# Kernel optimization log

Hardware: AMD Instinct MI355X
Metric: run time of the kernel (lower is better)

The kernel has to match this reference:

```python
import jax, jax.numpy as jnp
import numpy as np

N = 4096      # nodes
HID = 512     # hidden_size
HEADS = 8
DH = HID // HEADS
EPS = 1e-5    # BatchNorm eps


def setup_inputs() -> dict:
    key = jax.random.key(0)
    ks = jax.random.split(key, 16)
    h = jax.random.normal(ks[0], (N, HID), jnp.float32)
    # sparse adjacency (~degree 32) with self-loops so every row has a neighbor
    A = (jax.random.uniform(ks[1], (N, N)) < 0.008).astype(jnp.float32)
    A = jnp.maximum(A, jnp.eye(N, dtype=jnp.float32))
    w = lambda k, shp: jax.random.normal(k, shp, jnp.float32) * 0.02
    return {
        "A": A, "h": h,
        "Wq": w(ks[2], (HID, HID)), "bq": jnp.zeros((HID,), jnp.float32),
        "Wk": w(ks[3], (HID, HID)), "bk": jnp.zeros((HID,), jnp.float32),
        "Wv": w(ks[4], (HID, HID)), "bv": jnp.zeros((HID,), jnp.float32),
        "Wo": w(ks[5], (HID, HID)), "bo": jnp.zeros((HID,), jnp.float32),
        "bn1_g": jnp.ones((HID,), jnp.float32), "bn1_b": jnp.zeros((HID,), jnp.float32),
        "bn2_g": jnp.ones((HID,), jnp.float32), "bn2_b": jnp.zeros((HID,), jnp.float32),
        "W1": w(ks[6], (HID, 2 * HID)), "b1": jnp.zeros((2 * HID,), jnp.float32),
        "W2": w(ks[7], (2 * HID, HID)), "b2": jnp.zeros((HID,), jnp.float32),
    }


def _batchnorm(x, g, b):
    # BatchNorm1d training mode: stats over the node (batch) axis
    m = jnp.mean(x, axis=0)
    v = jnp.var(x, axis=0)
    return g * (x - m) * jax.lax.rsqrt(v + EPS) + b


def _layer(A, h, Wq, bq, Wk, bk, Wv, bv, Wo, bo,
           bn1_g, bn1_b, bn2_g, bn2_b, W1, b1, W2, b2):
    n = h.shape[0]
    q = (h @ Wq + bq).reshape(n, HEADS, DH)
    k = (h @ Wk + bk).reshape(n, HEADS, DH)
    v = (h @ Wv + bv).reshape(n, HEADS, DH)
    # scores [heads, n, m], masked by adjacency
    scores = jnp.einsum('nhd,mhd->hnm', q, k) / np.float32(np.sqrt(DH))
    scores = jnp.where(A[None, :, :] > 0, scores, jnp.float32(-1e9))
    attn = jax.nn.softmax(scores, axis=-1)
    o = jnp.einsum('hnm,mhd->nhd', attn, v).reshape(n, HID)
    h1 = o @ Wo + bo
    h = _batchnorm(h + h1, bn1_g, bn1_b)
    h2 = jax.nn.relu(h @ W1 + b1) @ W2 + b2
    return _batchnorm(h + h2, bn2_g, bn2_b)


def reference(A, h, Wq, bq, Wk, bk, Wv, bv, Wo, bo,
              bn1_g, bn1_b, bn2_g, bn2_b, W1, b1, W2, b2):
    return _layer(A, h, Wq, bq, Wk, bk, Wv, bv, Wo, bo,
                  bn1_g, bn1_b, bn2_g, bn2_b, W1, b1, W2, b2)
```

## Files before the change

kernel.cpp:

```cpp
#include <hip/hip_runtime.h>

#define N_NODES 4096
#define HID 512
#define HEADS 8
#define DH 64
#define EPS 1e-5f
#define MAXD 128

typedef __attribute__((ext_vector_type(8))) short bf16x8;
typedef __attribute__((ext_vector_type(4))) float f32x4;

__device__ __forceinline__ unsigned short f2bf(float f) {
    unsigned int u = __float_as_uint(f);
    unsigned int r = (u + 0x7FFFu + ((u >> 16) & 1u)) >> 16;
    return (unsigned short)r;
}
__device__ __forceinline__ float blo(unsigned int u) {
    return __uint_as_float(u << 16);
}
__device__ __forceinline__ float bhi(unsigned int u) {
    return __uint_as_float(u & 0xffff0000u);
}

__device__ __forceinline__ void gld_lds16(const void* g, void* l) {
    __builtin_amdgcn_global_load_lds(
        (const __attribute__((address_space(1))) unsigned int*)g,
        (__attribute__((address_space(3))) unsigned int*)l, 16, 0, 0);
}

template<int TM, int EPI>
__global__ __launch_bounds__(256) void gemm_bf16(
    const unsigned short* __restrict__ Xb, const unsigned short* __restrict__ Wt,
    const float* __restrict__ bias, const float* __restrict__ res,
    const unsigned short* __restrict__ resb,
    float* __restrict__ outf, unsigned short* __restrict__ outb,
    float* __restrict__ sum, float* __restrict__ sumsq,
    int K, int Nc)
{
    constexpr int WM = TM / 64;
    __shared__ __align__(16) unsigned short As[TM * 64];
    __shared__ __align__(16) unsigned short Bs[64 * 64];

    const int tid = threadIdx.x;
    const int lane = tid & 63;
    const int wv = tid >> 6;
    const int m0 = blockIdx.y * TM, n0 = blockIdx.x * 64;
    const int lc = lane & 15, lq = lane >> 4;
    const int rowbase = wv * (WM * 16);

    const int srow = tid >> 3;
    const int schunk = (tid & 7) ^ (srow & 7);
    unsigned short* ldsA = As + tid * 8;
    unsigned short* ldsB = Bs + tid * 8;
    const int rs0 = lq ^ (lc & 7);
    const int rs1 = (4 + lq) ^ (lc & 7);

    f32x4 acc[WM][4] = {};

    for (int k0 = 0; k0 < K; k0 += 64) {
        const unsigned short* gA = Xb + (size_t)(m0 + srow) * K + k0 + schunk * 8;
        const unsigned short* gB = Wt + (size_t)(n0 + srow) * K + k0 + schunk * 8;
        #pragma unroll
        for (int p = 0; p < TM / 32; ++p)
            gld_lds16(gA + (size_t)(p * 32) * K, ldsA + p * 2048);
        #pragma unroll
        for (int p = 0; p < 2; ++p)
            gld_lds16(gB + (size_t)(p * 32) * K, ldsB + p * 2048);
        __syncthreads();

        #pragma unroll
        for (int hh = 0; hh < 2; ++hh) {
            const int rs = hh ? rs1 : rs0;
            bf16x8 af[WM], bfr[4];
            #pragma unroll
            for (int i = 0; i < WM; ++i)
                af[i] = *(const bf16x8*)&As[(rowbase + i * 16 + lc) * 64 + rs * 8];
            #pragma unroll
            for (int j = 0; j < 4; ++j)
                bfr[j] = *(const bf16x8*)&Bs[(j * 16 + lc) * 64 + rs * 8];
            #pragma unroll
            for (int i = 0; i < WM; ++i)
                #pragma unroll
                for (int j = 0; j < 4; ++j)
                    acc[i][j] = __builtin_amdgcn_mfma_f32_16x16x32_bf16(af[i], bfr[j], acc[i][j], 0, 0, 0);
        }
        __syncthreads();
    }

    float cs[4] = {}, css[4] = {};
    #pragma unroll
    for (int i = 0; i < WM; ++i) {
        #pragma unroll
        for (int j = 0; j < 4; ++j) {
            const int gr0 = m0 + rowbase + i * 16 + lq * 4;
            const int gc = n0 + j * 16 + lc;
            const float bi = bias[gc];
            #pragma unroll
            for (int r = 0; r < 4; ++r) {
                float val = acc[i][j][r] + bi;
                size_t off = (size_t)(gr0 + r) * Nc + gc;
                if (EPI == 0)      outb[off] = f2bf(val);
                else if (EPI == 1) outb[off] = f2bf(fmaxf(val, 0.f));
                else {
                    if (EPI == 2) val += res[off];
                    else          val += blo((unsigned int)resb[off]);
                    outf[off] = val;
                    cs[j] += val; css[j] += val * val;
                }
            }
        }
    }
    if (EPI >= 2) {
        #pragma unroll
        for (int j = 0; j < 4; ++j) {
            float s = cs[j], ss = css[j];
            s += __shfl_xor(s, 16); s += __shfl_xor(s, 32);
            ss += __shfl_xor(ss, 16); ss += __shfl_xor(ss, 32);
            if (lq == 0) {
                const int gc = n0 + j * 16 + lc;
                atomicAdd(&sum[gc], s);
                atomicAdd(&sumsq[gc], ss);
            }
        }
    }
}

__global__ __launch_bounds__(256) void prep_all(
    const float* __restrict__ Wq, const float* __restrict__ Wk,
    const float* __restrict__ Wv, const float* __restrict__ Wo,
    const float* __restrict__ W1, const float* __restrict__ W2,
    const float* __restrict__ h,
    const float* __restrict__ bq, const float* __restrict__ bk,
    const float* __restrict__ bv,
    unsigned short* __restrict__ wqkvT, unsigned short* __restrict__ woT,
    unsigned short* __restrict__ w1T, unsigned short* __restrict__ w2T,
    unsigned int* __restrict__ hb, float* __restrict__ bqkv,
    float* __restrict__ st,
    const float* __restrict__ Adj, int* __restrict__ adjIdx,
    int* __restrict__ adjCnt)
{
    const int z = blockIdx.z;
    if (z < 6) {
        const float* in; unsigned short* out; int R, C;
        switch (z) {
            case 0: in = Wq; out = wqkvT;          R = 512;  C = 512;  break;
            case 1: in = Wk; out = wqkvT + 262144; R = 512;  C = 512;  break;
            case 2: in = Wv; out = wqkvT + 524288; R = 512;  C = 512;  break;
            case 3: in = Wo; out = woT;            R = 512;  C = 512;  break;
            case 4: in = W1; out = w1T;            R = 512;  C = 1024; break;
            default: in = W2; out = w2T;           R = 1024; C = 512;  break;
        }
        const int bc = blockIdx.x * 32, br = blockIdx.y * 32;
        if (bc >= C || br >= R) return;
        __shared__ float tile[32][33];
        const int tx = threadIdx.x & 31, ty = threadIdx.x >> 5;
        #pragma unroll
        for (int r = ty; r < 32; r += 8)
            tile[r][tx] = in[(size_t)(br + r) * C + bc + tx];
        __syncthreads();
        #pragma unroll
        for (int r = ty; r < 32; r += 8)
            out[(size_t)(bc + r) * R + br + tx] = f2bf(tile[tx][r]);
    } else if (z == 6) {
        const int blk = blockIdx.y * 32 + blockIdx.x;
        const int i = blk * 512 + threadIdx.x * 2;
        const float4* in4 = (const float4*)h;
        #pragma unroll
        for (int u = 0; u < 2; ++u) {
            float4 f = in4[i + u];
            hb[(i + u) * 2]     = (unsigned int)f2bf(f.x) | ((unsigned int)f2bf(f.y) << 16);
            hb[(i + u) * 2 + 1] = (unsigned int)f2bf(f.z) | ((unsigned int)f2bf(f.w) << 16);
        }
    } else if (z == 7) {
        const int blk = blockIdx.y * 32 + blockIdx.x;
        const int i = blk * 256 + threadIdx.x;
        if (i < 1536) bqkv[i] = i < 512 ? bq[i] : (i < 1024 ? bk[i - 512] : bv[i - 1024]);
        if (i < 2048) st[i] = 0.0f;
    } else {
        const int tid = threadIdx.x;
        const int lane = tid & 63;
        const int wv4 = tid >> 6;
        __shared__ int s_cnt[4];
        const unsigned long long lt = (1ull << lane) - 1ull;
        const int blk = blockIdx.y * 32 + blockIdx.x;
        #pragma unroll
        for (int it = 0; it < 4; ++it) {
            const int n = blk * 4 + it;
            const float4* r4 = (const float4*)(Adj + (size_t)n * N_NODES);
            float4 av[4];
            #pragma unroll
            for (int t = 0; t < 4; ++t)
                av[t] = r4[wv4 * 256 + t * 64 + lane];
            int cnt = 0;
            #pragma unroll
            for (int t = 0; t < 4; ++t) {
                #pragma unroll
                for (int b = 0; b < 4; ++b) {
                    float vb = (b == 0) ? av[t].x : (b == 1) ? av[t].y : (b == 2) ? av[t].z : av[t].w;
                    cnt += __popcll(__ballot(vb > 0.0f));
                }
            }
            if (lane == 0) s_cnt[wv4] = cnt;
            __syncthreads();
            int base = 0, total = 0;
            #pragma unroll
            for (int w = 0; w < 4; ++w) {
                if (w < wv4) base += s_cnt[w];
                total += s_cnt[w];
            }
            #pragma unroll
            for (int t = 0; t < 4; ++t) {
                #pragma unroll
                for (int b = 0; b < 4; ++b) {
                    float vb = (b == 0) ? av[t].x : (b == 1) ? av[t].y : (b == 2) ? av[t].z : av[t].w;
                    unsigned long long m = __ballot(vb > 0.0f);
                    if (vb > 0.0f) {
                        int p = base + __popcll(m & lt);
                        if (p < MAXD) adjIdx[n * MAXD + p] = wv4 * 1024 + t * 256 + lane * 4 + b;
                    }
                    base += __popcll(m);
                }
            }
            if (tid == 0) adjCnt[n] = total < MAXD ? total : MAXD;
            __syncthreads();
        }
    }
}

__global__ __launch_bounds__(256) void sparse_attn6(
    const int* __restrict__ adjIdx, const int* __restrict__ adjCnt,
    const unsigned short* __restrict__ qkv, unsigned short* __restrict__ o)
{
    const int n = blockIdx.x;
    const int tid = threadIdx.x;
    const int wv = tid >> 6, lane = tid & 63;

    __shared__ int s_idx[MAXD];
    __shared__ float s_p[8][MAXD];

    const int d = adjCnt[n];
    if (tid < d) s_idx[tid] = adjIdx[n * MAXD + tid];
    __syncthreads();

    const int jl = lane >> 3;
    const int dgs = lane & 7;
    const int jl2 = lane >> 4;
    const int dga = lane & 15;
    const int h0 = wv, h1 = wv + 4;

    const unsigned short* qp = qkv + (size_t)n * 1536 + dgs * 8;
    uint4 qa = *(const uint4*)(qp + h0 * 64);
    uint4 qb = *(const uint4*)(qp + h1 * 64);
    const float a0 = blo(qa.x), a1 = bhi(qa.x), a2 = blo(qa.y), a3 = bhi(qa.y);
    const float a4 = blo(qa.z), a5 = bhi(qa.z), a6 = blo(qa.w), a7 = bhi(qa.w);
    const float b0 = blo(qb.x), b1 = bhi(qb.x), b2 = blo(qb.y), b3 = bhi(qb.y);
    const float b4 = blo(qb.z), b5 = bhi(qb.z), b6 = blo(qb.w), b7 = bhi(qb.w);

    uint4 ka = {0, 0, 0, 0}, kb = {0, 0, 0, 0};
    if (jl < d) {
        const unsigned short* p = qkv + (size_t)s_idx[jl] * 1536 + 512 + dgs * 8;
        ka = *(const uint4*)(p + h0 * 64);
        kb = *(const uint4*)(p + h1 * 64);
    }
    for (int j0 = 0; j0 < d; j0 += 8) {
        const uint4 ca = ka, cb = kb;
        const int jn = j0 + 8 + jl;
        if (jn < d) {
            const unsigned short* p = qkv + (size_t)s_idx[jn] * 1536 + 512 + dgs * 8;
            ka = *(const uint4*)(p + h0 * 64);
            kb = *(const uint4*)(p + h1 * 64);
        }
        const int jc = j0 + jl;
        float s0 = 0.f, s1 = 0.f;
        if (jc < d) {
            s0 = a0 * blo(ca.x) + a1 * bhi(ca.x) + a2 * blo(ca.y) + a3 * bhi(ca.y)
               + a4 * blo(ca.z) + a5 * bhi(ca.z) + a6 * blo(ca.w) + a7 * bhi(ca.w);
            s1 = b0 * blo(cb.x) + b1 * bhi(cb.x) + b2 * blo(cb.y) + b3 * bhi(cb.y)
               + b4 * blo(cb.z) + b5 * bhi(cb.z) + b6 * blo(cb.w) + b7 * bhi(cb.w);
        }
        s0 += __shfl_xor(s0, 1); s1 += __shfl_xor(s1, 1);
        s0 += __shfl_xor(s0, 2); s1 += __shfl_xor(s1, 2);
        s0 += __shfl_xor(s0, 4); s1 += __shfl_xor(s1, 4);
        if (dgs == 0 && jc < d) {
            s_p[h0][jc] = s0 * 0.125f;
            s_p[h1][jc] = s1 * 0.125f;
        }
    }

    float inv0, inv1;
    #pragma unroll
    for (int hh = 0; hh < 2; ++hh) {
        float* sp = s_p[hh ? h1 : h0];
        float mx = -1e30f;
        for (int j = lane; j < d; j += 64) mx = fmaxf(mx, sp[j]);
        #pragma unroll
        for (int off = 32; off; off >>= 1) mx = fmaxf(mx, __shfl_xor(mx, off));
        float sum = 0.f;
        for (int j = lane; j < d; j += 64) {
            float e = __expf(sp[j] - mx);
            sp[j] = e;
            sum += e;
        }
        #pragma unroll
        for (int off = 32; off; off >>= 1) sum += __shfl_xor(sum, off);
        if (hh) inv1 = 1.0f / sum; else inv0 = 1.0f / sum;
    }

    float x0 = 0.f, x1 = 0.f, x2 = 0.f, x3 = 0.f;
    float y0 = 0.f, y1 = 0.f, y2 = 0.f, y3 = 0.f;
    uint2 va = {0, 0}, vb = {0, 0};
    if (jl2 < d) {
        const unsigned short* p = qkv + (size_t)s_idx[jl2] * 1536 + 1024 + dga * 4;
        va = *(const uint2*)(p + h0 * 64);
        vb = *(const uint2*)(p + h1 * 64);
    }
    for (int j0 = 0; j0 < d; j0 += 4) {
        const uint2 ca = va, cb = vb;
        const int jn = j0 + 4 + jl2;
        if (jn < d) {
            const unsigned short* p = qkv + (size_t)s_idx[jn] * 1536 + 1024 + dga * 4;
            va = *(const uint2*)(p + h0 * 64);
            vb = *(const uint2*)(p + h1 * 64);
        }
        const int jc = j0 + jl2;
        if (jc < d) {
            const float p0 = s_p[h0][jc], p1 = s_p[h1][jc];
            x0 += p0 * blo(ca.x); x1 += p0 * bhi(ca.x);
            x2 += p0 * blo(ca.y); x3 += p0 * bhi(ca.y);
            y0 += p1 * blo(cb.x); y1 += p1 * bhi(cb.x);
            y2 += p1 * blo(cb.y); y3 += p1 * bhi(cb.y);
        }
    }
    x0 += __shfl_xor(x0, 16); x0 += __shfl_xor(x0, 32);
    x1 += __shfl_xor(x1, 16); x1 += __shfl_xor(x1, 32);
    x2 += __shfl_xor(x2, 16); x2 += __shfl_xor(x2, 32);
    x3 += __shfl_xor(x3, 16); x3 += __shfl_xor(x3, 32);
    y0 += __shfl_xor(y0, 16); y0 += __shfl_xor(y0, 32);
    y1 += __shfl_xor(y1, 16); y1 += __shfl_xor(y1, 32);
    y2 += __shfl_xor(y2, 16); y2 += __shfl_xor(y2, 32);
    y3 += __shfl_xor(y3, 16); y3 += __shfl_xor(y3, 32);
    if (jl2 == 0) {
        uint2 w0, w1;
        w0.x = (unsigned int)f2bf(x0 * inv0) | ((unsigned int)f2bf(x1 * inv0) << 16);
        w0.y = (unsigned int)f2bf(x2 * inv0) | ((unsigned int)f2bf(x3 * inv0) << 16);
        w1.x = (unsigned int)f2bf(y0 * inv1) | ((unsigned int)f2bf(y1 * inv1) << 16);
        w1.y = (unsigned int)f2bf(y2 * inv1) | ((unsigned int)f2bf(y3 * inv1) << 16);
        *(uint2*)(o + (size_t)n * 512 + h0 * 64 + dga * 4) = w0;
        *(uint2*)(o + (size_t)n * 512 + h1 * 64 + dga * 4) = w1;
    }
}

__global__ __launch_bounds__(256) void bn_apply4(
    const float4* __restrict__ x, const float* __restrict__ sum,
    const float* __restrict__ sumsq, const float* __restrict__ g,
    const float* __restrict__ b, float4* __restrict__ yf,
    uint2* __restrict__ yb)
{
    const int i = blockIdx.x * 256 + threadIdx.x;
    const int c4 = i & 127;
    const float4 s4 = ((const float4*)sum)[c4];
    const float4 q4 = ((const float4*)sumsq)[c4];
    const float4 g4 = ((const float4*)g)[c4];
    const float4 b4 = ((const float4*)b)[c4];
    const float4 xv = x[i];
    const float kN = 1.0f / N_NODES;
    float4 r;
    { float m = s4.x * kN; r.x = g4.x * (xv.x - m) * rsqrtf(q4.x * kN - m * m + EPS) + b4.x; }
    { float m = s4.y * kN; r.y = g4.y * (xv.y - m) * rsqrtf(q4.y * kN - m * m + EPS) + b4.y; }
    { float m = s4.z * kN; r.z = g4.z * (xv.z - m) * rsqrtf(q4.z * kN - m * m + EPS) + b4.z; }
    { float m = s4.w * kN; r.w = g4.w * (xv.w - m) * rsqrtf(q4.w * kN - m * m + EPS) + b4.w; }
    if (yf) yf[i] = r;
    if (yb) {
        uint2 p;
        p.x = (unsigned int)f2bf(r.x) | ((unsigned int)f2bf(r.y) << 16);
        p.y = (unsigned int)f2bf(r.z) | ((unsigned int)f2bf(r.w) << 16);
        yb[i] = p;
    }
}


extern "C" void kernel_launch(void* const* d_in, const int* in_sizes, int n_in,
                              void* d_out, int out_size, void* d_ws, size_t ws_size,
                              hipStream_t stream)
{
    const float* A   = (const float*)d_in[0];
    const float* h   = (const float*)d_in[1];
    const float* Wq  = (const float*)d_in[2];
    const float* bq  = (const float*)d_in[3];
    const float* Wk  = (const float*)d_in[4];
    const float* bk  = (const float*)d_in[5];
    const float* Wv  = (const float*)d_in[6];
    const float* bv  = (const float*)d_in[7];
    const float* Wo  = (const float*)d_in[8];
    const float* bo  = (const float*)d_in[9];
    const float* g1  = (const float*)d_in[10];
    const float* b1g = (const float*)d_in[11];
    const float* g2  = (const float*)d_in[12];
    const float* b2g = (const float*)d_in[13];
    const float* W1  = (const float*)d_in[14];
    const float* b1  = (const float*)d_in[15];
    const float* W2  = (const float*)d_in[16];
    const float* b2  = (const float*)d_in[17];
    float* out = (float*)d_out;

    float* ws = (float*)d_ws;
    unsigned short* hb    = (unsigned short*)(ws);
    unsigned short* qkvb  = (unsigned short*)(ws + 1048576);
    unsigned short* o_bf  = (unsigned short*)(ws + 4194304);
    unsigned short* wqkvT = (unsigned short*)(ws + 5242880);
    unsigned short* woT   = (unsigned short*)(ws + 5636096);
    unsigned short* w1T   = (unsigned short*)(ws + 5767168);
    unsigned short* w2T   = (unsigned short*)(ws + 6029312);
    unsigned short* t_b   = (unsigned short*)(ws + 6291456);
    float* x1   = ws + 8388608;
    float* x2   = ws + 10485760;
    unsigned short* xb1_b = (unsigned short*)(ws + 12582912);
    float* bqkv = ws + 13631488;
    float* st   = ws + 13633024;
    int* adjIdx = (int*)(ws + 6291456);
    int* adjCnt = (int*)(ws + 6815744);

    prep_all<<<dim3(32, 32, 9), dim3(256), 0, stream>>>(
        Wq, Wk, Wv, Wo, W1, W2, h, bq, bk, bv,
        wqkvT, woT, w1T, w2T, (unsigned int*)hb, bqkv, st,
        A, adjIdx, adjCnt);

    gemm_bf16<128, 0><<<dim3(24, 32), dim3(256), 0, stream>>>(
        hb, wqkvT, bqkv, nullptr, nullptr, nullptr, qkvb, nullptr, nullptr, 512, 1536);

    sparse_attn6<<<dim3(N_NODES), dim3(256), 0, stream>>>(adjIdx, adjCnt, qkvb, o_bf);

    gemm_bf16<64, 2><<<dim3(8, 64), dim3(256), 0, stream>>>(
        o_bf, woT, bo, h, nullptr, x1, nullptr, st, st + 512, 512, 512);

    bn_apply4<<<dim3(2048), dim3(256), 0, stream>>>(
        (const float4*)x1, st, st + 512, g1, b1g, nullptr, (uint2*)xb1_b);

    gemm_bf16<128, 1><<<dim3(16, 32), dim3(256), 0, stream>>>(
        xb1_b, w1T, b1, nullptr, nullptr, nullptr, t_b, nullptr, nullptr, 512, 1024);

    gemm_bf16<64, 3><<<dim3(8, 64), dim3(256), 0, stream>>>(
        t_b, w2T, b2, nullptr, xb1_b, x2, nullptr, st + 1024, st + 1536, 1024, 512);

    bn_apply4<<<dim3(2048), dim3(256), 0, stream>>>(
        (const float4*)x2, st + 1024, st + 1536, g2, b2g, (float4*)out, nullptr);

    (void)in_sizes; (void)n_in; (void)out_size; (void)ws_size;
}
```

Before: 237.6 us.

## Triple-buffer GEMM LDS tiles with two-stage async prefetch

Restructures the bf16 MFMA GEMM main loop to use three LDS buffers, issuing global-to-LDS loads two K-tiles ahead and waiting with explicit vmcnt counters plus a single barrier per iteration. It also raises wave priority around the MFMA section. This aims to hide global load latency behind compute and drop the second barrier. In exchange it triples LDS use, which may lower occupancy, and it relies on the hand-written vmcnt values being correct.

```diff
diff --git a/kernel.cpp b/kernel.cpp
--- a/kernel.cpp
+++ b/kernel.cpp
@@ -38,8 +38,9 @@
     int K, int Nc)
 {
     constexpr int WM = TM / 64;
-    __shared__ __align__(16) unsigned short As[TM * 64];
-    __shared__ __align__(16) unsigned short Bs[64 * 64];
+    constexpr int G  = TM / 32 + 2;
+    __shared__ __align__(16) unsigned short As[3][TM * 64];
+    __shared__ __align__(16) unsigned short Bs[3][64 * 64];
 
     const int tid = threadIdx.x;
     const int lane = tid & 63;
@@ -50,41 +51,65 @@
 
     const int srow = tid >> 3;
     const int schunk = (tid & 7) ^ (srow & 7);
-    unsigned short* ldsA = As + tid * 8;
-    unsigned short* ldsB = Bs + tid * 8;
     const int rs0 = lq ^ (lc & 7);
     const int rs1 = (4 + lq) ^ (lc & 7);
 
+    const unsigned short* gA = Xb + (size_t)(m0 + srow) * K + schunk * 8;
+    const unsigned short* gB = Wt + (size_t)(n0 + srow) * K + schunk * 8;
+
     f32x4 acc[WM][4] = {};
 
-    for (int k0 = 0; k0 < K; k0 += 64) {
-        const unsigned short* gA = Xb + (size_t)(m0 + srow) * K + k0 + schunk * 8;
-        const unsigned short* gB = Wt + (size_t)(n0 + srow) * K + k0 + schunk * 8;
-        #pragma unroll
-        for (int p = 0; p < TM / 32; ++p)
-            gld_lds16(gA + (size_t)(p * 32) * K, ldsA + p * 2048);
-        #pragma unroll
-        for (int p = 0; p < 2; ++p)
-            gld_lds16(gB + (size_t)(p * 32) * K, ldsB + p * 2048);
-        __syncthreads();
-
+    const int nt = K >> 6;
+
+    #pragma unroll
+    for (int p = 0; p < TM / 32; ++p)
+        gld_lds16(gA + (size_t)(p * 32) * K, As[0] + tid * 8 + p * 2048);
+    #pragma unroll
+    for (int p = 0; p < 2; ++p)
+        gld_lds16(gB + (size_t)(p * 32) * K, Bs[0] + tid * 8 + p * 2048);
+    #pragma unroll
+    for (int p = 0; p < TM / 32; ++p)
+        gld_lds16(gA + 64 + (size_t)(p * 32) * K, As[1] + tid * 8 + p * 2048);
+    #pragma unroll
+    for (int p = 0; p < 2; ++p)
+        gld_lds16(gB + 64 + (size_t)(p * 32) * K, Bs[1] + tid * 8 + p * 2048);
+
+    for (int t = 0; t < nt; ++t) {
+        if (t == nt - 1) asm volatile("s_waitcnt vmcnt(0)" ::: "memory");
+        else             asm volatile("s_waitcnt vmcnt(%0)" :: "i"(G) : "memory");
+        __builtin_amdgcn_s_barrier();
+
+        if (t + 2 < nt) {
+            const int b2 = (t + 2) % 3;
+            const int koff = (t + 2) * 64;
+            #pragma unroll
+            for (int p = 0; p < TM / 32; ++p)
+                gld_lds16(gA + koff + (size_t)(p * 32) * K, As[b2] + tid * 8 + p * 2048);
+            #pragma unroll
+            for (int p = 0; p < 2; ++p)
+                gld_lds16(gB + koff + (size_t)(p * 32) * K, Bs[b2] + tid * 8 + p * 2048);
+        }
+
+        const unsigned short* Ab = As[t % 3];
+        const unsigned short* Bb = Bs[t % 3];
+        __builtin_amdgcn_s_setprio(1);
         #pragma unroll
         for (int hh = 0; hh < 2; ++hh) {
             const int rs = hh ? rs1 : rs0;
             bf16x8 af[WM], bfr[4];
             #pragma unroll
             for (int i = 0; i < WM; ++i)
-                af[i] = *(const bf16x8*)&As[(rowbase + i * 16 + lc) * 64 + rs * 8];
+                af[i] = *(const bf16x8*)&Ab[(rowbase + i * 16 + lc) * 64 + rs * 8];
             #pragma unroll
             for (int j = 0; j < 4; ++j)
-                bfr[j] = *(const bf16x8*)&Bs[(j * 16 + lc) * 64 + rs * 8];
+                bfr[j] = *(const bf16x8*)&Bb[(j * 16 + lc) * 64 + rs * 8];
             #pragma unroll
             for (int i = 0; i < WM; ++i)
                 #pragma unroll
                 for (int j = 0; j < 4; ++j)
                     acc[i][j] = __builtin_amdgcn_mfma_f32_16x16x32_bf16(af[i], bfr[j], acc[i][j], 0, 0, 0);
         }
-        __syncthreads();
+        __builtin_amdgcn_s_setprio(0);
     }
 
     float cs[4] = {}, css[4] = {};
```

New measurement: 239.1 us. Within noise of the previous version (+0.7%).

## Fuse post-attention GEMMs and batchnorms into one cooperative kernel with grid syncs

Applied to the files above, without the earlier changes.

Replaces the five launches after attention (Wo GEMM, BN1 apply, W1 GEMM, W2 GEMM, BN2 apply) with one cooperative kernel of 512 blocks. The stages are separated by grid-wide syncs and each block walks its tile indices by hand. The goal is to remove the launch overhead and gaps between launches. In exchange, the kernel is limited to a grid that fits on the device at the same time (launch_bounds 256,2), each grid.sync has a cost, and the W1 stage loses flexibility in its tile shape.

```diff
diff --git a/kernel.cpp b/kernel.cpp
--- a/kernel.cpp
+++ b/kernel.cpp
@@ -1,4 +1,7 @@
 #include <hip/hip_runtime.h>
+#include <hip/hip_cooperative_groups.h>
+
+namespace cg = cooperative_groups;
 
 #define N_NODES 4096
 #define HID 512
@@ -29,22 +32,20 @@
 }
 
 template<int TM, int EPI>
-__global__ __launch_bounds__(256) void gemm_bf16(
+__device__ __forceinline__ void gemm_tile(
     const unsigned short* __restrict__ Xb, const unsigned short* __restrict__ Wt,
     const float* __restrict__ bias, const float* __restrict__ res,
     const unsigned short* __restrict__ resb,
     float* __restrict__ outf, unsigned short* __restrict__ outb,
     float* __restrict__ sum, float* __restrict__ sumsq,
-    int K, int Nc)
+    int K, int Nc, int bx, int by,
+    unsigned short* As, unsigned short* Bs)
 {
     constexpr int WM = TM / 64;
-    __shared__ __align__(16) unsigned short As[TM * 64];
-    __shared__ __align__(16) unsigned short Bs[64 * 64];
-
     const int tid = threadIdx.x;
     const int lane = tid & 63;
     const int wv = tid >> 6;
-    const int m0 = blockIdx.y * TM, n0 = blockIdx.x * 64;
+    const int m0 = by * TM, n0 = bx * 64;
     const int lc = lane & 15, lq = lane >> 4;
     const int rowbase = wv * (WM * 16);
 
@@ -125,238 +126,24 @@
     }
 }
 
-__global__ __launch_bounds__(256) void prep_all(
-    const float* __restrict__ Wq, const float* __restrict__ Wk,
-    const float* __restrict__ Wv, const float* __restrict__ Wo,
-    const float* __restrict__ W1, const float* __restrict__ W2,
-    const float* __restrict__ h,
-    const float* __restrict__ bq, const float* __restrict__ bk,
-    const float* __restrict__ bv,
-    unsigned short* __restrict__ wqkvT, unsigned short* __restrict__ woT,
-    unsigned short* __restrict__ w1T, unsigned short* __restrict__ w2T,
-    unsigned int* __restrict__ hb, float* __restrict__ bqkv,
-    float* __restrict__ st,
-    const float* __restrict__ Adj, int* __restrict__ adjIdx,
-    int* __restrict__ adjCnt)
-{
-    const int z = blockIdx.z;
-    if (z < 6) {
-        const float* in; unsigned short* out; int R, C;
-        switch (z) {
-            case 0: in = Wq; out = wqkvT;          R = 512;  C = 512;  break;
-            case 1: in = Wk; out = wqkvT + 262144; R = 512;  C = 512;  break;
-            case 2: in = Wv; out = wqkvT + 524288; R = 512;  C = 512;  break;
-            case 3: in = Wo; out = woT;            R = 512;  C = 512;  break;
-            case 4: in = W1; out = w1T;            R = 512;  C = 1024; break;
-            default: in = W2; out = w2T;           R = 1024; C = 512;  break;
-        }
-        const int bc = blockIdx.x * 32, br = blockIdx.y * 32;
-        if (bc >= C || br >= R) return;
-        __shared__ float tile[32][33];
-        const int tx = threadIdx.x & 31, ty = threadIdx.x >> 5;
-        #pragma unroll
-        for (int r = ty; r < 32; r += 8)
-            tile[r][tx] = in[(size_t)(br + r) * C + bc + tx];
-        __syncthreads();
-        #pragma unroll
-        for (int r = ty; r < 32; r += 8)
-            out[(size_t)(bc + r) * R + br + tx] = f2bf(tile[tx][r]);
-    } else if (z == 6) {
-        const int blk = blockIdx.y * 32 + blockIdx.x;
-        const int i = blk * 512 + threadIdx.x * 2;
-        const float4* in4 = (const float4*)h;
-        #pragma unroll
-        for (int u = 0; u < 2; ++u) {
-            float4 f = in4[i + u];
-            hb[(i + u) * 2]     = (unsigned int)f2bf(f.x) | ((unsigned int)f2bf(f.y) << 16);
-            hb[(i + u) * 2 + 1] = (unsigned int)f2bf(f.z) | ((unsigned int)f2bf(f.w) << 16);
-        }
-    } else if (z == 7) {
-        const int blk = blockIdx.y * 32 + blockIdx.x;
-        const int i = blk * 256 + threadIdx.x;
-        if (i < 1536) bqkv[i] = i < 512 ? bq[i] : (i < 1024 ? bk[i - 512] : bv[i - 1024]);
-        if (i < 2048) st[i] = 0.0f;
-    } else {
-        const int tid = threadIdx.x;
-        const int lane = tid & 63;
-        const int wv4 = tid >> 6;
-        __shared__ int s_cnt[4];
-        const unsigned long long lt = (1ull << lane) - 1ull;
-        const int blk = blockIdx.y * 32 + blockIdx.x;
-        #pragma unroll
-        for (int it = 0; it < 4; ++it) {
-            const int n = blk * 4 + it;
-            const float4* r4 = (const float4*)(Adj + (size_t)n * N_NODES);
-            float4 av[4];
-            #pragma unroll
-            for (int t = 0; t < 4; ++t)
-                av[t] = r4[wv4 * 256 + t * 64 + lane];
-            int cnt = 0;
-            #pragma unroll
-            for (int t = 0; t < 4; ++t) {
-                #pragma unroll
-                for (int b = 0; b < 4; ++b) {
-                    float vb = (b == 0) ? av[t].x : (b == 1) ? av[t].y : (b == 2) ? av[t].z : av[t].w;
-                    cnt += __popcll(__ballot(vb > 0.0f));
-                }
-            }
-            if (lane == 0) s_cnt[wv4] = cnt;
-            __syncthreads();
-            int base = 0, total = 0;
-            #pragma unroll
-            for (int w = 0; w < 4; ++w) {
-                if (w < wv4) base += s_cnt[w];
-                total += s_cnt[w];
-            }
-            #pragma unroll
-            for (int t = 0; t < 4; ++t) {
-                #pragma unroll
-                for (int b = 0; b < 4; ++b) {
-                    float vb = (b == 0) ? av[t].x : (b == 1) ? av[t].y : (b == 2) ? av[t].z : av[t].w;
-                    unsigned long long m = __ballot(vb > 0.0f);
-                    if (vb > 0.0f) {
-                        int p = base + __popcll(m & lt);
-                        if (p < MAXD) adjIdx[n * MAXD + p] = wv4 * 1024 + t * 256 + lane * 4 + b;
-                    }
-                    base += __popcll(m);
-                }
-            }
-            if (tid == 0) adjCnt[n] = total < MAXD ? total : MAXD;
-            __syncthreads();
-        }
-    }
-}
-
-__global__ __launch_bounds__(256) void sparse_attn6(
-    const int* __restrict__ adjIdx, const int* __restrict__ adjCnt,
-    const unsigned short* __restrict__ qkv, unsigned short* __restrict__ o)
-{
-    const int n = blockIdx.x;
-    const int tid = threadIdx.x;
-    const int wv = tid >> 6, lane = tid & 63;
-
-    __shared__ int s_idx[MAXD];
-    __shared__ float s_p[8][MAXD];
-
-    const int d = adjCnt[n];
-    if (tid < d) s_idx[tid] = adjIdx[n * MAXD + tid];
-    __syncthreads();
-
-    const int jl = lane >> 3;
-    const int dgs = lane & 7;
-    const int jl2 = lane >> 4;
-    const int dga = lane & 15;
-    const int h0 = wv, h1 = wv + 4;
-
-    const unsigned short* qp = qkv + (size_t)n * 1536 + dgs * 8;
-    uint4 qa = *(const uint4*)(qp + h0 * 64);
-    uint4 qb = *(const uint4*)(qp + h1 * 64);
-    const float a0 = blo(qa.x), a1 = bhi(qa.x), a2 = blo(qa.y), a3 = bhi(qa.y);
-    const float a4 = blo(qa.z), a5 = bhi(qa.z), a6 = blo(qa.w), a7 = bhi(qa.w);
-    const float b0 = blo(qb.x), b1 = bhi(qb.x), b2 = blo(qb.y), b3 = bhi(qb.y);
-    const float b4 = blo(qb.z), b5 = bhi(qb.z), b6 = blo(qb.w), b7 = bhi(qb.w);
-
-    uint4 ka = {0, 0, 0, 0}, kb = {0, 0, 0, 0};
-    if (jl < d) {
-        const unsigned short* p = qkv + (size_t)s_idx[jl] * 1536 + 512 + dgs * 8;
-        ka = *(const uint4*)(p + h0 * 64);
-        kb = *(const uint4*)(p + h1 * 64);
-    }
-    for (int j0 = 0; j0 < d; j0 += 8) {
-        const uint4 ca = ka, cb = kb;
-        const int jn = j0 + 8 + jl;
-        if (jn < d) {
-            const unsigned short* p = qkv + (size_t)s_idx[jn] * 1536 + 512 + dgs * 8;
-            ka = *(const uint4*)(p + h0 * 64);
-            kb = *(const uint4*)(p + h1 * 64);
-        }
-        const int jc = j0 + jl;
-        float s0 = 0.f, s1 = 0.f;
-        if (jc < d) {
-            s0 = a0 * blo(ca.x) + a1 * bhi(ca.x) + a2 * blo(ca.y) + a3 * bhi(ca.y)
-               + a4 * blo(ca.z) + a5 * bhi(ca.z) + a6 * blo(ca.w) + a7 * bhi(ca.w);
-            s1 = b0 * blo(cb.x) + b1 * bhi(cb.x) + b2 * blo(cb.y) + b3 * bhi(cb.y)
-               + b4 * blo(cb.z) + b5 * bhi(cb.z) + b6 * blo(cb.w) + b7 * bhi(cb.w);
-        }
-        s0 += __shfl_xor(s0, 1); s1 += __shfl_xor(s1, 1);
-        s0 += __shfl_xor(s0, 2); s1 += __shfl_xor(s1, 2);
-        s0 += __shfl_xor(s0, 4); s1 += __shfl_xor(s1, 4);
-        if (dgs == 0 && jc < d) {
-            s_p[h0][jc] = s0 * 0.125f;
-            s_p[h1][jc] = s1 * 0.125f;
-        }
-    }
-
-    float inv0, inv1;
-    #pragma unroll
-    for (int hh = 0; hh < 2; ++hh) {
-        float* sp = s_p[hh ? h1 : h0];
-        float mx = -1e30f;
-        for (int j = lane; j < d; j += 64) mx = fmaxf(mx, sp[j]);
-        #pragma unroll
-        for (int off = 32; off; off >>= 1) mx = fmaxf(mx, __shfl_xor(mx, off));
-        float sum = 0.f;
-        for (int j = lane; j < d; j += 64) {
-            float e = __expf(sp[j] - mx);
-            sp[j] = e;
-            sum += e;
-        }
-        #pragma unroll
-        for (int off = 32; off; off >>= 1) sum += __shfl_xor(sum, off);
-        if (hh) inv1 = 1.0f / sum; else inv0 = 1.0f / sum;
-    }
-
-    float x0 = 0.f, x1 = 0.f, x2 = 0.f, x3 = 0.f;
-    float y0 = 0.f, y1 = 0.f, y2 = 0.f, y3 = 0.f;
-    uint2 va = {0, 0}, vb = {0, 0};
-    if (jl2 < d) {
-        const unsigned short* p = qkv + (size_t)s_idx[jl2] * 1536 + 1024 + dga * 4;
-        va = *(const uint2*)(p + h0 * 64);
-        vb = *(const uint2*)(p + h1 * 64);
-    }
-    for (int j0 = 0; j0 < d; j0 += 4) {
-        const uint2 ca = va, cb = vb;
-        const int jn = j0 + 4 + jl2;
-        if (jn < d) {
-            const unsigned short* p = qkv + (size_t)s_idx[jn] * 1536 + 1024 + dga * 4;
-            va = *(const uint2*)(p + h0 * 64);
-            vb = *(const uint2*)(p + h1 * 64);
-        }
-        const int jc = j0 + jl2;
-        if (jc < d) {
-            const float p0 = s_p[h0][jc], p1 = s_p[h1][jc];
-            x0 += p0 * blo(ca.x); x1 += p0 * bhi(ca.x);
-            x2 += p0 * blo(ca.y); x3 += p0 * bhi(ca.y);
-            y0 += p1 * blo(cb.x); y1 += p1 * bhi(cb.x);
-            y2 += p1 * blo(cb.y); y3 += p1 * bhi(cb.y);
-        }
-    }
-    x0 += __shfl_xor(x0, 16); x0 += __shfl_xor(x0, 32);
-    x1 += __shfl_xor(x1, 16); x1 += __shfl_xor(x1, 32);
-    x2 += __shfl_xor(x2, 16); x2 += __shfl_xor(x2, 32);
-    x3 += __shfl_xor(x3, 16); x3 += __shfl_xor(x3, 32);
-    y0 += __shfl_xor(y0, 16); y0 += __shfl_xor(y0, 32);
-    y1 += __shfl_xor(y1, 16); y1 += __shfl_xor(y1, 32);
-    y2 += __shfl_xor(y2, 16); y2 += __shfl_xor(y2, 32);
-    y3 += __shfl_xor(y3, 16); y3 += __shfl_xor(y3, 32);
-    if (jl2 == 0) {
-        uint2 w0, w1;
-        w0.x = (unsigned int)f2bf(x0 * inv0) | ((unsigned int)f2bf(x1 * inv0) << 16);
-        w0.y = (unsigned int)f2bf(x2 * inv0) | ((unsigned int)f2bf(x3 * inv0) << 16);
-        w1.x = (unsigned int)f2bf(y0 * inv1) | ((unsigned int)f2bf(y1 * inv1) << 16);
-        w1.y = (unsigned int)f2bf(y2 * inv1) | ((unsigned int)f2bf(y3 * inv1) << 16);
-        *(uint2*)(o + (size_t)n * 512 + h0 * 64 + dga * 4) = w0;
-        *(uint2*)(o + (size_t)n * 512 + h1 * 64 + dga * 4) = w1;
-    }
-}
-
-__global__ __launch_bounds__(256) void bn_apply4(
+template<int TM, int EPI>
+__global__ __launch_bounds__(256) void gemm_bf16(
+    const unsigned short* __restrict__ Xb, const unsigned short* __restrict__ Wt,
+    const float* __restrict__ bias,
+    unsigned short* __restrict__ outb, int K, int Nc)
+{
+    __shared__ __align__(16) unsigned short As[TM * 64];
+    __shared__ __align__(16) unsigned short Bs[64 * 64];
+    gemm_tile<TM, EPI>(Xb, Wt, bias, nullptr, nullptr, nullptr, outb,
+                       nullptr, nullptr, K, Nc, blockIdx.x, blockIdx.y, As, Bs);
+}
+
+__device__ __forceinline__ void bn_item(
     const float4* __restrict__ x, const float* __restrict__ sum,
     const float* __restrict__ sumsq, const float* __restrict__ g,
     const float* __restrict__ b, float4* __restrict__ yf,
-    uint2* __restrict__ yb)
-{
-    const int i = blockIdx.x * 256 + threadIdx.x;
+    uint2* __restrict__ yb, int i)
+{
     const int c4 = i & 127;
     const float4 s4 = ((const float4*)sum)[c4];
     const float4 q4 = ((const float4*)sumsq)[c4];
@@ -375,6 +162,275 @@
         p.x = (unsigned int)f2bf(r.x) | ((unsigned int)f2bf(r.y) << 16);
         p.y = (unsigned int)f2bf(r.z) | ((unsigned int)f2bf(r.w) << 16);
         yb[i] = p;
+    }
+}
+
+__global__ __launch_bounds__(256, 2) void megaB(
+    const unsigned short* __restrict__ o_bf, const unsigned short* __restrict__ woT,
+    const float* __restrict__ bo, const float* __restrict__ h,
+    float* __restrict__ x1,
+    const float* __restrict__ g1, const float* __restrict__ b1g,
+    unsigned short* __restrict__ xb1_b,
+    const unsigned short* __restrict__ w1T, const float* __restrict__ b1,
+    unsigned short* __restrict__ t_b,
+    const unsigned short* __restrict__ w2T, const float* __restrict__ b2,
+    float* __restrict__ x2,
+    const float* __restrict__ g2, const float* __restrict__ b2g,
+    float* __restrict__ out, float* __restrict__ st)
+{
+    __shared__ __align__(16) unsigned short smem[128 * 64 + 64 * 64];
+    cg::grid_group grid = cg::this_grid();
+    const int bid = blockIdx.x;
+    const int tid = threadIdx.x;
+
+    gemm_tile<64, 2>(o_bf, woT, bo, h, nullptr, x1, nullptr, st, st + 512,
+                     512, 512, bid & 7, bid >> 3, smem, smem + 64 * 64);
+    grid.sync();
+
+    #pragma unroll
+    for (int it = 0; it < 4; ++it)
+        bn_item((const float4*)x1, st, st + 512, g1, b1g, nullptr,
+                (uint2*)xb1_b, (it * 512 + bid) * 256 + tid);
+    grid.sync();
+
+    gemm_tile<128, 1>(xb1_b, w1T, b1, nullptr, nullptr, nullptr, t_b,
+                      nullptr, nullptr, 512, 1024, bid & 15, bid >> 4,
+                      smem, smem + 128 * 64);
+    grid.sync();
+
+    gemm_tile<64, 3>(t_b, w2T, b2, nullptr, xb1_b, x2, nullptr,
+                     st + 1024, st + 1536, 1024, 512, bid & 7, bid >> 3,
+                     smem, smem + 64 * 64);
+    grid.sync();
+
+    #pragma unroll
+    for (int it = 0; it < 4; ++it)
+        bn_item((const float4*)x2, st + 1024, st + 1536, g2, b2g,
+                (float4*)out, nullptr, (it * 512 + bid) * 256 + tid);
+}
+
+__global__ __launch_bounds__(256) void prep_all(
+    const float* __restrict__ Wq, const float* __restrict__ Wk,
+    const float* __restrict__ Wv, const float* __restrict__ Wo,
+    const float* __restrict__ W1, const float* __restrict__ W2,
+    const float* __restrict__ h,
+    const float* __restrict__ bq, const float* __restrict__ bk,
+    const float* __restrict__ bv,
+    unsigned short* __restrict__ wqkvT, unsigned short* __restrict__ woT,
+    unsigned short* __restrict__ w1T, unsigned short* __restrict__ w2T,
+    unsigned int* __restrict__ hb, float* __restrict__ bqkv,
+    float* __restrict__ st,
+    const float* __restrict__ Adj, int* __restrict__ adjIdx,
+    int* __restrict__ adjCnt)
+{
+    const int z = blockIdx.z;
+    if (z < 6) {
+        const float* in; unsigned short* out; int R, C;
+        switch (z) {
+            case 0: in = Wq; out = wqkvT;          R = 512;  C = 512;  break;
+            case 1: in = Wk; out = wqkvT + 262144; R = 512;  C = 512;  break;
+            case 2: in = Wv; out = wqkvT + 524288; R = 512;  C = 512;  break;
+            case 3: in = Wo; out = woT;            R = 512;  C = 512;  break;
+            case 4: in = W1; out = w1T;            R = 512;  C = 1024; break;
+            default: in = W2; out = w2T;           R = 1024; C = 512;  break;
+        }
+        const int bc = blockIdx.x * 32, br = blockIdx.y * 32;
+        if (bc >= C || br >= R) return;
+        __shared__ float tile[32][33];
+        const int tx = threadIdx.x & 31, ty = threadIdx.x >> 5;
+        #pragma unroll
+        for (int r = ty; r < 32; r += 8)
+            tile[r][tx] = in[(size_t)(br + r) * C + bc + tx];
+        __syncthreads();
+        #pragma unroll
+        for (int r = ty; r < 32; r += 8)
+            out[(size_t)(bc + r) * R + br + tx] = f2bf(tile[tx][r]);
+    } else if (z == 6) {
+        const int blk = blockIdx.y * 32 + blockIdx.x;
+        const int i = blk * 512 + threadIdx.x * 2;
+        const float4* in4 = (const float4*)h;
+        #pragma unroll
+        for (int u = 0; u < 2; ++u) {
+            float4 f = in4[i + u];
+            hb[(i + u) * 2]     = (unsigned int)f2bf(f.x) | ((unsigned int)f2bf(f.y) << 16);
+            hb[(i + u) * 2 + 1] = (unsigned int)f2bf(f.z) | ((unsigned int)f2bf(f.w) << 16);
+        }
+    } else if (z == 7) {
+        const int blk = blockIdx.y * 32 + blockIdx.x;
+        const int i = blk * 256 + threadIdx.x;
+        if (i < 1536) bqkv[i] = i < 512 ? bq[i] : (i < 1024 ? bk[i - 512] : bv[i - 1024]);
+        if (i < 2048) st[i] = 0.0f;
+    } else {
+        const int tid = threadIdx.x;
+        const int lane = tid & 63;
+        const int wv4 = tid >> 6;
+        __shared__ int s_cnt[4];
+        const unsigned long long lt = (1ull << lane) - 1ull;
+        const int blk = blockIdx.y * 32 + blockIdx.x;
+        #pragma unroll
+        for (int it = 0; it < 4; ++it) {
+            const int n = blk * 4 + it;
+            const float4* r4 = (const float4*)(Adj + (size_t)n * N_NODES);
+            float4 av[4];
+            #pragma unroll
+            for (int t = 0; t < 4; ++t)
+                av[t] = r4[wv4 * 256 + t * 64 + lane];
+            int cnt = 0;
+            #pragma unroll
+            for (int t = 0; t < 4; ++t) {
+                #pragma unroll
+                for (int b = 0; b < 4; ++b) {
+                    float vb = (b == 0) ? av[t].x : (b == 1) ? av[t].y : (b == 2) ? av[t].z : av[t].w;
+                    cnt += __popcll(__ballot(vb > 0.0f));
+                }
+            }
+            if (lane == 0) s_cnt[wv4] = cnt;
+            __syncthreads();
+            int base = 0, total = 0;
+            #pragma unroll
+            for (int w = 0; w < 4; ++w) {
+                if (w < wv4) base += s_cnt[w];
+                total += s_cnt[w];
+            }
+            #pragma unroll
+            for (int t = 0; t < 4; ++t) {
+                #pragma unroll
+                for (int b = 0; b < 4; ++b) {
+                    float vb = (b == 0) ? av[t].x : (b == 1) ? av[t].y : (b == 2) ? av[t].z : av[t].w;
+                    unsigned long long m = __ballot(vb > 0.0f);
+                    if (vb > 0.0f) {
+                        int p = base + __popcll(m & lt);
+                        if (p < MAXD) adjIdx[n * MAXD + p] = wv4 * 1024 + t * 256 + lane * 4 + b;
+                    }
+                    base += __popcll(m);
+                }
+            }
+            if (tid == 0) adjCnt[n] = total < MAXD ? total : MAXD;
+            __syncthreads();
+        }
+    }
+}
+
+__global__ __launch_bounds__(256) void sparse_attn6(
+    const int* __restrict__ adjIdx, const int* __restrict__ adjCnt,
+    const unsigned short* __restrict__ qkv, unsigned short* __restrict__ o)
+{
+    const int n = blockIdx.x;
+    const int tid = threadIdx.x;
+    const int wv = tid >> 6, lane = tid & 63;
+
+    __shared__ int s_idx[MAXD];
+    __shared__ float s_p[8][MAXD];
+
+    const int d = adjCnt[n];
+    if (tid < d) s_idx[tid] = adjIdx[n * MAXD + tid];
+    __syncthreads();
+
+    const int jl = lane >> 3;
+    const int dgs = lane & 7;
+    const int jl2 = lane >> 4;
+    const int dga = lane & 15;
+    const int h0 = wv, h1 = wv + 4;
+
+    const unsigned short* qp = qkv + (size_t)n * 1536 + dgs * 8;
+    uint4 qa = *(const uint4*)(qp + h0 * 64);
+    uint4 qb = *(const uint4*)(qp + h1 * 64);
+    const float a0 = blo(qa.x), a1 = bhi(qa.x), a2 = blo(qa.y), a3 = bhi(qa.y);
+    const float a4 = blo(qa.z), a5 = bhi(qa.z), a6 = blo(qa.w), a7 = bhi(qa.w);
+    const float b0 = blo(qb.x), b1 = bhi(qb.x), b2 = blo(qb.y), b3 = bhi(qb.y);
+    const float b4 = blo(qb.z), b5 = bhi(qb.z), b6 = blo(qb.w), b7 = bhi(qb.w);
+
+    uint4 ka = {0, 0, 0, 0}, kb = {0, 0, 0, 0};
+    if (jl < d) {
+        const unsigned short* p = qkv + (size_t)s_idx[jl] * 1536 + 512 + dgs * 8;
+        ka = *(const uint4*)(p + h0 * 64);
+        kb = *(const uint4*)(p + h1 * 64);
+    }
+    for (int j0 = 0; j0 < d; j0 += 8) {
+        const uint4 ca = ka, cb = kb;
+        const int jn = j0 + 8 + jl;
+        if (jn < d) {
+            const unsigned short* p = qkv + (size_t)s_idx[jn] * 1536 + 512 + dgs * 8;
+            ka = *(const uint4*)(p + h0 * 64);
+            kb = *(const uint4*)(p + h1 * 64);
+        }
+        const int jc = j0 + jl;
+        float s0 = 0.f, s1 = 0.f;
+        if (jc < d) {
+            s0 = a0 * blo(ca.x) + a1 * bhi(ca.x) + a2 * blo(ca.y) + a3 * bhi(ca.y)
+               + a4 * blo(ca.z) + a5 * bhi(ca.z) + a6 * blo(ca.w) + a7 * bhi(ca.w);
+            s1 = b0 * blo(cb.x) + b1 * bhi(cb.x) + b2 * blo(cb.y) + b3 * bhi(cb.y)
+               + b4 * blo(cb.z) + b5 * bhi(cb.z) + b6 * blo(cb.w) + b7 * bhi(cb.w);
+        }
+        s0 += __shfl_xor(s0, 1); s1 += __shfl_xor(s1, 1);
+        s0 += __shfl_xor(s0, 2); s1 += __shfl_xor(s1, 2);
+        s0 += __shfl_xor(s0, 4); s1 += __shfl_xor(s1, 4);
+        if (dgs == 0 && jc < d) {
+            s_p[h0][jc] = s0 * 0.125f;
+            s_p[h1][jc] = s1 * 0.125f;
+        }
+    }
+
+    float inv0, inv1;
+    #pragma unroll
+    for (int hh = 0; hh < 2; ++hh) {
+        float* sp = s_p[hh ? h1 : h0];
+        float mx = -1e30f;
+        for (int j = lane; j < d; j += 64) mx = fmaxf(mx, sp[j]);
+        #pragma unroll
+        for (int off = 32; off; off >>= 1) mx = fmaxf(mx, __shfl_xor(mx, off));
+        float sum = 0.f;
+        for (int j = lane; j < d; j += 64) {
+            float e = __expf(sp[j] - mx);
+            sp[j] = e;
+            sum += e;
+        }
+        #pragma unroll
+        for (int off = 32; off; off >>= 1) sum += __shfl_xor(sum, off);
+        if (hh) inv1 = 1.0f / sum; else inv0 = 1.0f / sum;
+    }
+
+    float x0 = 0.f, x1 = 0.f, x2 = 0.f, x3 = 0.f;
+    float y0 = 0.f, y1 = 0.f, y2 = 0.f, y3 = 0.f;
+    uint2 va = {0, 0}, vb = {0, 0};
+    if (jl2 < d) {
+        const unsigned short* p = qkv + (size_t)s_idx[jl2] * 1536 + 1024 + dga * 4;
+        va = *(const uint2*)(p + h0 * 64);
+        vb = *(const uint2*)(p + h1 * 64);
+    }
+    for (int j0 = 0; j0 < d; j0 += 4) {
+        const uint2 ca = va, cb = vb;
+        const int jn = j0 + 4 + jl2;
+        if (jn < d) {
+            const unsigned short* p = qkv + (size_t)s_idx[jn] * 1536 + 1024 + dga * 4;
+            va = *(const uint2*)(p + h0 * 64);
+            vb = *(const uint2*)(p + h1 * 64);
+        }
+        const int jc = j0 + jl2;
+        if (jc < d) {
+            const float p0 = s_p[h0][jc], p1 = s_p[h1][jc];
+            x0 += p0 * blo(ca.x); x1 += p0 * bhi(ca.x);
+            x2 += p0 * blo(ca.y); x3 += p0 * bhi(ca.y);
+            y0 += p1 * blo(cb.x); y1 += p1 * bhi(cb.x);
+            y2 += p1 * blo(cb.y); y3 += p1 * bhi(cb.y);
+        }
+    }
+    x0 += __shfl_xor(x0, 16); x0 += __shfl_xor(x0, 32);
+    x1 += __shfl_xor(x1, 16); x1 += __shfl_xor(x1, 32);
+    x2 += __shfl_xor(x2, 16); x2 += __shfl_xor(x2, 32);
+    x3 += __shfl_xor(x3, 16); x3 += __shfl_xor(x3, 32);
+    y0 += __shfl_xor(y0, 16); y0 += __shfl_xor(y0, 32);
+    y1 += __shfl_xor(y1, 16); y1 += __shfl_xor(y1, 32);
+    y2 += __shfl_xor(y2, 16); y2 += __shfl_xor(y2, 32);
+    y3 += __shfl_xor(y3, 16); y3 += __shfl_xor(y3, 32);
+    if (jl2 == 0) {
+        uint2 w0, w1;
+        w0.x = (unsigned int)f2bf(x0 * inv0) | ((unsigned int)f2bf(x1 * inv0) << 16);
+        w0.y = (unsigned int)f2bf(x2 * inv0) | ((unsigned int)f2bf(x3 * inv0) << 16);
+        w1.x = (unsigned int)f2bf(y0 * inv1) | ((unsigned int)f2bf(y1 * inv1) << 16);
+        w1.y = (unsigned int)f2bf(y2 * inv1) | ((unsigned int)f2bf(y3 * inv1) << 16);
+        *(uint2*)(o + (size_t)n * 512 + h0 * 64 + dga * 4) = w0;
+        *(uint2*)(o + (size_t)n * 512 + h1 * 64 + dga * 4) = w1;
     }
 }
 
@@ -426,24 +482,27 @@
         A, adjIdx, adjCnt);
 
     gemm_bf16<128, 0><<<dim3(24, 32), dim3(256), 0, stream>>>(
-        hb, wqkvT, bqkv, nullptr, nullptr, nullptr, qkvb, nullptr, nullptr, 512, 1536);
+        hb, wqkvT, bqkv, qkvb, 512, 1536);
 
     sparse_attn6<<<dim3(N_NODES), dim3(256), 0, stream>>>(adjIdx, adjCnt, qkvb, o_bf);
 
-    gemm_bf16<64, 2><<<dim3(8, 64), dim3(256), 0, stream>>>(
-        o_bf, woT, bo, h, nullptr, x1, nullptr, st, st + 512, 512, 512);
-
-    bn_apply4<<<dim3(2048), dim3(256), 0, stream>>>(
-        (const float4*)x1, st, st + 512, g1, b1g, nullptr, (uint2*)xb1_b);
-
-    gemm_bf16<128, 1><<<dim3(16, 32), dim3(256), 0, stream>>>(
-        xb1_b, w1T, b1, nullptr, nullptr, nullptr, t_b, nullptr, nullptr, 512, 1024);
-
-    gemm_bf16<64, 3><<<dim3(8, 64), dim3(256), 0, stream>>>(
-        t_b, w2T, b2, nullptr, xb1_b, x2, nullptr, st + 1024, st + 1536, 1024, 512);
-
-    bn_apply4<<<dim3(2048), dim3(256), 0, stream>>>(
-        (const float4*)x2, st + 1024, st + 1536, g2, b2g, (float4*)out, nullptr);
+    {
+        const unsigned short* a0 = o_bf;  const unsigned short* a1 = woT;
+        const float* a2 = bo;             const float* a3 = h;
+        float* a4 = x1;
+        const float* a5 = g1;             const float* a6 = b1g;
+        unsigned short* a7 = xb1_b;
+        const unsigned short* a8 = w1T;   const float* a9 = b1;
+        unsigned short* a10 = t_b;
+        const unsigned short* a11 = w2T;  const float* a12 = b2;
+        float* a13 = x2;
+        const float* a14 = g2;            const float* a15 = b2g;
+        float* a16 = out;                 float* a17 = st;
+        void* margs[] = { &a0, &a1, &a2, &a3, &a4, &a5, &a6, &a7, &a8, &a9,
+                          &a10, &a11, &a12, &a13, &a14, &a15, &a16, &a17 };
+        hipLaunchCooperativeKernel((void*)megaB, dim3(512), dim3(256),
+                                   margs, 0, stream);
+    }
 
     (void)in_sizes; (void)n_in; (void)out_size; (void)ws_size;
 }
```

After: 498.8 us. +110.0%, slower.

## Fuse first BatchNorm apply into FFN1 A-load and FFN2 residual epilogue

Applied to the files above, without the earlier changes.

Drops the standalone bn_apply kernel that turned x1 into a normalized bf16 copy. A new FFN1 GEMM kernel reads fp32 x1 directly, applies the per-channel BN scale and shift (precomputed into shared memory), converts to bf16 while staging the A tile, and applies the ReLU epilogue. The FFN2 epilogue recomputes the BN affine per column to rebuild the normalized residual from fp32 x1. This removes one launch and a round trip through an intermediate buffer. In exchange, FFN1 now loads fp32 activations synchronously instead of using async global-to-LDS bf16 loads, and each FFN1 block recomputes the BN coefficients for all 512 channels.

```diff
diff --git a/kernel.cpp b/kernel.cpp
--- a/kernel.cpp
+++ b/kernel.cpp
@@ -32,10 +32,11 @@
 __global__ __launch_bounds__(256) void gemm_bf16(
     const unsigned short* __restrict__ Xb, const unsigned short* __restrict__ Wt,
     const float* __restrict__ bias, const float* __restrict__ res,
-    const unsigned short* __restrict__ resb,
     float* __restrict__ outf, unsigned short* __restrict__ outb,
     float* __restrict__ sum, float* __restrict__ sumsq,
-    int K, int Nc)
+    int K, int Nc,
+    const float* __restrict__ bnG, const float* __restrict__ bnB,
+    const float* __restrict__ bnSt)
 {
     constexpr int WM = TM / 64;
     __shared__ __align__(16) unsigned short As[TM * 64];
@@ -95,6 +96,13 @@
             const int gr0 = m0 + rowbase + i * 16 + lq * 4;
             const int gc = n0 + j * 16 + lc;
             const float bi = bias[gc];
+            float aj = 0.f, bj = 0.f;
+            if (EPI == 4) {
+                float mm = bnSt[gc] * (1.0f / N_NODES);
+                float rr = rsqrtf(bnSt[512 + gc] * (1.0f / N_NODES) - mm * mm + EPS);
+                aj = bnG[gc] * rr;
+                bj = fmaf(-mm, aj, bnB[gc]);
+            }
             #pragma unroll
             for (int r = 0; r < 4; ++r) {
                 float val = acc[i][j][r] + bi;
@@ -103,7 +111,7 @@
                 else if (EPI == 1) outb[off] = f2bf(fmaxf(val, 0.f));
                 else {
                     if (EPI == 2) val += res[off];
-                    else          val += blo((unsigned int)resb[off]);
+                    else          val += fmaf(res[off], aj, bj);
                     outf[off] = val;
                     cs[j] += val; css[j] += val * val;
                 }
@@ -120,6 +128,105 @@
                 const int gc = n0 + j * 16 + lc;
                 atomicAdd(&sum[gc], s);
                 atomicAdd(&sumsq[gc], ss);
+            }
+        }
+    }
+}
+
+__global__ __launch_bounds__(256) void gemm_ffn1(
+    const float* __restrict__ x1, const unsigned short* __restrict__ Wt,
+    const float* __restrict__ bias, const float* __restrict__ g,
+    const float* __restrict__ bb, const float* __restrict__ st,
+    unsigned short* __restrict__ outb)
+{
+    constexpr int TM = 128, WM = 2;
+    __shared__ __align__(16) unsigned short As[TM * 64];
+    __shared__ __align__(16) unsigned short Bs[64 * 64];
+    __shared__ float sA[512];
+    __shared__ float sB[512];
+
+    const int tid = threadIdx.x;
+    const int lane = tid & 63;
+    const int wv = tid >> 6;
+    const int m0 = blockIdx.y * TM, n0 = blockIdx.x * 64;
+    const int lc = lane & 15, lq = lane >> 4;
+    const int rowbase = wv * (WM * 16);
+    const int srow = tid >> 3;
+    const int schunk = (tid & 7) ^ (srow & 7);
+    unsigned short* ldsB = Bs + tid * 8;
+    const int rs0 = lq ^ (lc & 7);
+    const int rs1 = (4 + lq) ^ (lc & 7);
+
+    for (int c = tid; c < 512; c += 256) {
+        float m = st[c] * (1.0f / N_NODES);
+        float r = rsqrtf(st[512 + c] * (1.0f / N_NODES) - m * m + EPS);
+        float a = g[c] * r;
+        sA[c] = a;
+        sB[c] = fmaf(-m, a, bb[c]);
+    }
+    __syncthreads();
+
+    f32x4 acc[WM][4] = {};
+
+    for (int k0 = 0; k0 < 512; k0 += 64) {
+        const unsigned short* gB = Wt + (size_t)(n0 + srow) * 512 + k0 + schunk * 8;
+        #pragma unroll
+        for (int p = 0; p < 2; ++p)
+            gld_lds16(gB + (size_t)(p * 32) * 512, ldsB + p * 2048);
+
+        const int c0 = k0 + schunk * 8;
+        const float4 a0 = *(const float4*)&sA[c0];
+        const float4 a1 = *(const float4*)&sA[c0 + 4];
+        const float4 o0 = *(const float4*)&sB[c0];
+        const float4 o1 = *(const float4*)&sB[c0 + 4];
+        #pragma unroll
+        for (int p = 0; p < 4; ++p) {
+            const float* gx = x1 + (size_t)(m0 + p * 32 + srow) * 512 + c0;
+            const float4 v0 = *(const float4*)gx;
+            const float4 v1 = *(const float4*)(gx + 4);
+            const float y0 = fmaf(v0.x, a0.x, o0.x), y1 = fmaf(v0.y, a0.y, o0.y);
+            const float y2 = fmaf(v0.z, a0.z, o0.z), y3 = fmaf(v0.w, a0.w, o0.w);
+            const float y4 = fmaf(v1.x, a1.x, o1.x), y5 = fmaf(v1.y, a1.y, o1.y);
+            const float y6 = fmaf(v1.z, a1.z, o1.z), y7 = fmaf(v1.w, a1.w, o1.w);
+            uint4 w;
+            w.x = (unsigned int)f2bf(y0) | ((unsigned int)f2bf(y1) << 16);
+            w.y = (unsigned int)f2bf(y2) | ((unsigned int)f2bf(y3) << 16);
+            w.z = (unsigned int)f2bf(y4) | ((unsigned int)f2bf(y5) << 16);
+            w.w = (unsigned int)f2bf(y6) | ((unsigned int)f2bf(y7) << 16);
+            *(uint4*)&As[tid * 8 + p * 2048] = w;
+        }
+        __syncthreads();
+
+        #pragma unroll
+        for (int hh = 0; hh < 2; ++hh) {
+            const int rs = hh ? rs1 : rs0;
+            bf16x8 af[WM], bfr[4];
+            #pragma unroll
+            for (int i = 0; i < WM; ++i)
+                af[i] = *(const bf16x8*)&As[(rowbase + i * 16 + lc) * 64 + rs * 8];
+            #pragma unroll
+            for (int j = 0; j < 4; ++j)
+                bfr[j] = *(const bf16x8*)&Bs[(j * 16 + lc) * 64 + rs * 8];
+            #pragma unroll
+            for (int i = 0; i < WM; ++i)
+                #pragma unroll
+                for (int j = 0; j < 4; ++j)
+                    acc[i][j] = __builtin_amdgcn_mfma_f32_16x16x32_bf16(af[i], bfr[j], acc[i][j], 0, 0, 0);
+        }
+        __syncthreads();
+    }
+
+    #pragma unroll
+    for (int i = 0; i < WM; ++i) {
+        #pragma unroll
+        for (int j = 0; j < 4; ++j) {
+            const int gr0 = m0 + rowbase + i * 16 + lq * 4;
+            const int gc = n0 + j * 16 + lc;
+            const float bi = bias[gc];
+            #pragma unroll
+            for (int r = 0; r < 4; ++r) {
+                float val = acc[i][j][r] + bi;
+                outb[(size_t)(gr0 + r) * 1024 + gc] = f2bf(fmaxf(val, 0.f));
             }
         }
     }
@@ -353,8 +460,7 @@
 __global__ __launch_bounds__(256) void bn_apply4(
     const float4* __restrict__ x, const float* __restrict__ sum,
     const float* __restrict__ sumsq, const float* __restrict__ g,
-    const float* __restrict__ b, float4* __restrict__ yf,
-    uint2* __restrict__ yb)
+    const float* __restrict__ b, float4* __restrict__ yf)
 {
     const int i = blockIdx.x * 256 + threadIdx.x;
     const int c4 = i & 127;
@@ -369,13 +475,7 @@
     { float m = s4.y * kN; r.y = g4.y * (xv.y - m) * rsqrtf(q4.y * kN - m * m + EPS) + b4.y; }
     { float m = s4.z * kN; r.z = g4.z * (xv.z - m) * rsqrtf(q4.z * kN - m * m + EPS) + b4.z; }
     { float m = s4.w * kN; r.w = g4.w * (xv.w - m) * rsqrtf(q4.w * kN - m * m + EPS) + b4.w; }
-    if (yf) yf[i] = r;
-    if (yb) {
-        uint2 p;
-        p.x = (unsigned int)f2bf(r.x) | ((unsigned int)f2bf(r.y) << 16);
-        p.y = (unsigned int)f2bf(r.z) | ((unsigned int)f2bf(r.w) << 16);
-        yb[i] = p;
-    }
+    yf[i] = r;
 }
 
 
@@ -414,7 +514,6 @@
     unsigned short* t_b   = (unsigned short*)(ws + 6291456);
     float* x1   = ws + 8388608;
     float* x2   = ws + 10485760;
-    unsigned short* xb1_b = (unsigned short*)(ws + 12582912);
     float* bqkv = ws + 13631488;
     float* st   = ws + 13633024;
     int* adjIdx = (int*)(ws + 6291456);
@@ -426,24 +525,24 @@
         A, adjIdx, adjCnt);
 
     gemm_bf16<128, 0><<<dim3(24, 32), dim3(256), 0, stream>>>(
-        hb, wqkvT, bqkv, nullptr, nullptr, nullptr, qkvb, nullptr, nullptr, 512, 1536);
+        hb, wqkvT, bqkv, nullptr, nullptr, qkvb, nullptr, nullptr,
+        512, 1536, nullptr, nullptr, nullptr);
 
     sparse_attn6<<<dim3(N_NODES), dim3(256), 0, stream>>>(adjIdx, adjCnt, qkvb, o_bf);
 
     gemm_bf16<64, 2><<<dim3(8, 64), dim3(256), 0, stream>>>(
-        o_bf, woT, bo, h, nullptr, x1, nullptr, st, st + 512, 512, 512);
+        o_bf, woT, bo, h, x1, nullptr, st, st + 512,
+        512, 512, nullptr, nullptr, nullptr);
+
+    gemm_ffn1<<<dim3(16, 32), dim3(256), 0, stream>>>(
+        x1, w1T, b1, g1, b1g, st, t_b);
+
+    gemm_bf16<64, 4><<<dim3(8, 64), dim3(256), 0, stream>>>(
+        t_b, w2T, b2, x1, x2, nullptr, st + 1024, st + 1536,
+        1024, 512, g1, b1g, st);
 
     bn_apply4<<<dim3(2048), dim3(256), 0, stream>>>(
-        (const float4*)x1, st, st + 512, g1, b1g, nullptr, (uint2*)xb1_b);
-
-    gemm_bf16<128, 1><<<dim3(16, 32), dim3(256), 0, stream>>>(
-        xb1_b, w1T, b1, nullptr, nullptr, nullptr, t_b, nullptr, nullptr, 512, 1024);
-
-    gemm_bf16<64, 3><<<dim3(8, 64), dim3(256), 0, stream>>>(
-        t_b, w2T, b2, nullptr, xb1_b, x2, nullptr, st + 1024, st + 1536, 1024, 512);
-
-    bn_apply4<<<dim3(2048), dim3(256), 0, stream>>>(
-        (const float4*)x2, st + 1024, st + 1536, g2, b2g, (float4*)out, nullptr);
+        (const float4*)x2, st + 1024, st + 1536, g2, b2g, (float4*)out);
 
     (void)in_sizes; (void)n_in; (void)out_size; (void)ws_size;
 }
```

Result: slower. 247.8 us (+4.3%).
